# Kernel optimization log

Measured on AMD Instinct MI355X. Metric: run time of the kernel, lower is better.

The kernel has to match this reference:

```python
import jax, jax.numpy as jnp
import numpy as np

B, S, D, F = 8, 2048, 256, 8

def setup_inputs() -> dict:
    key = jax.random.key(0)
    ks = jax.random.split(key, 7)
    hidden_states = jax.random.normal(ks[0], (B, S, D), dtype=jnp.float32)
    # flat indices into zero-prepended [1 + B*S, D] token table; 0 = padding row
    select_idx = jax.random.randint(ks[1], (B, S, F), 0, B * S + 1, dtype=jnp.int32)
    word_mask = jax.random.randint(ks[2], (B, S), 0, 2, dtype=jnp.int32)
    W1 = jax.random.normal(ks[3], (D, D), dtype=jnp.float32) * (1.0 / np.sqrt(D))
    b1 = jax.random.normal(ks[4], (D,), dtype=jnp.float32) * 0.02
    w2 = jax.random.normal(ks[5], (D,), dtype=jnp.float32) * (1.0 / np.sqrt(D))
    b2 = jax.random.normal(ks[6], (1,), dtype=jnp.float32) * 0.02
    return {"hidden_states": hidden_states, "select_idx": select_idx,
            "word_mask": word_mask, "W1": W1, "b1": b1, "w2": w2, "b2": b2}

def reference(hidden_states, select_idx, word_mask, W1, b1, w2, b2):
    b, s, d = hidden_states.shape
    h = jnp.tanh(hidden_states.reshape(-1, d) @ W1.T + b1)          # [B*S, D]
    h = jnp.concatenate([jnp.zeros((1, d), h.dtype), h], axis=0)    # zero padding row at index 0
    g = h[select_idx.reshape(-1)]                                    # gather: [B*S*F, D]
    g = g.reshape(b * s, -1, d).max(axis=1)                          # AdaptiveMaxPool1d(1) over word occurrences
    scores = (g @ w2 + b2[0]).reshape(b, s)                          # w2 linear -> [B, S]
    neg = -10000.0 * (1.0 - word_mask.astype(jnp.float32))
    return scores.astype(jnp.float32) + neg
```

## Files before the change

kernel.cpp:

```cpp
#include <hip/hip_runtime.h>
#include <hip/hip_bf16.h>
#include <math.h>

#define BB 8
#define SS 2048
#define DD 256
#define FF 8
#define NTOK (BB*SS)

typedef __bf16 bf16x8 __attribute__((ext_vector_type(8)));
typedef float  f32x4  __attribute__((ext_vector_type(4)));
typedef float  f32x2  __attribute__((ext_vector_type(2)));

#define BM 32
#define WCH 64
#define NCH (DD/WCH)

__device__ __forceinline__ unsigned pack2_bf16(float a, float b) {
    return (__float_as_uint(a) >> 16) | (__float_as_uint(b) & 0xFFFF0000u);
}
__device__ __forceinline__ float fast_tanh(float x) {
    float e = __expf(2.0f * x);
    return 1.0f - 2.0f * __builtin_amdgcn_rcpf(e + 1.0f);
}
__device__ __forceinline__ unsigned char f32_to_fp8(float v) {
    return (unsigned char)(__builtin_amdgcn_cvt_pk_fp8_f32(v, v, 0, false) & 0xFF);
}

__global__ __launch_bounds__(512, 4) void gemm_tanh_kernel(
    const float* __restrict__ x, const float* __restrict__ W1,
    const float* __restrict__ b1, unsigned char* __restrict__ table)
{
    __shared__ __align__(16) unsigned short xs[BM * DD];
    __shared__ __align__(16) unsigned short wb[WCH * DD];

    const int tid  = threadIdx.x;
    const int bx   = blockIdx.x;
    const int tok0 = bx * BM;

    if (bx == 0 && tid < 64) ((unsigned int*)table)[tid] = 0u;

    const int wave = tid >> 6, lane = tid & 63;
    const int mf = wave >> 2;
    const int nf = wave & 3;
    const int lr = lane & 15;
    const int kg = lane >> 4;
    const int sw = lr & 7;

    f32x4 wr[8];
    auto wload = [&](int nc) {
        #pragma unroll
        for (int p = 0; p < 8; ++p) {
            int s = p * 512 + tid;
            int row = s >> 6, k4 = s & 63;
            wr[p] = *(const f32x4*)&W1[(size_t)(nc * WCH + row) * DD + k4 * 4];
        }
    };
    auto wstore = [&]() {
        #pragma unroll
        for (int p = 0; p < 8; ++p) {
            int s = p * 512 + tid;
            int row = s >> 6, k4 = s & 63;
            uint2 pk;
            pk.x = pack2_bf16(wr[p].x, wr[p].y);
            pk.y = pack2_bf16(wr[p].z, wr[p].w);
            int gp = (k4 >> 1) ^ (row & 7);
            *(uint2*)&wb[row * DD + gp * 8 + (k4 & 1) * 4] = pk;
        }
    };

    wload(0);

    #pragma unroll
    for (int p = 0; p < 4; ++p) {
        int s = p * 512 + tid;
        int row = s >> 6, k4 = s & 63;
        f32x4 v = *(const f32x4*)&x[(size_t)(tok0 + row) * DD + k4 * 4];
        uint2 pk;
        pk.x = pack2_bf16(v.x, v.y);
        pk.y = pack2_bf16(v.z, v.w);
        int gp = (k4 >> 1) ^ (row & 7);
        *(uint2*)&xs[row * DD + gp * 8 + (k4 & 1) * 4] = pk;
    }

    wstore();
    __syncthreads();

    f32x4 acc[NCH];
    #pragma unroll
    for (int nc = 0; nc < NCH; ++nc) acc[nc] = (f32x4){0.f, 0.f, 0.f, 0.f};

    const int arow = mf * 16 + lr;
    const int nrow = nf * 16 + lr;

    #pragma unroll
    for (int nc = 0; nc < NCH; ++nc) {
        if (nc + 1 < NCH) wload(nc + 1);

        #pragma unroll
        for (int c = 0; c < 8; ++c) {
            int gp8 = ((c * 4 + kg) ^ sw) * 8;
            bf16x8 af = *(const bf16x8*)&xs[arow * DD + gp8];
            bf16x8 bf = *(const bf16x8*)&wb[nrow * DD + gp8];
            acc[nc] = __builtin_amdgcn_mfma_f32_16x16x32_bf16(af, bf, acc[nc], 0, 0, 0);
        }
        __syncthreads();
        if (nc + 1 < NCH) {
            wstore();
            __syncthreads();
        }
    }

    float bj[NCH];
    #pragma unroll
    for (int nc = 0; nc < NCH; ++nc) bj[nc] = b1[nc * WCH + nf * 16 + lr];

    unsigned char* sc = (unsigned char*)&xs[0];
    #pragma unroll
    for (int nc = 0; nc < NCH; ++nc) {
        #pragma unroll
        for (int r = 0; r < 4; ++r) {
            int row = mf * 16 + kg * 4 + r;
            int col = nc * WCH + nf * 16 + lr;
            float v = fast_tanh(acc[nc][r] + bj[nc]);
            sc[row * 272 + col] = f32_to_fp8(v);
        }
    }
    __syncthreads();
    {
        int row = tid >> 4;
        int off = (tid & 15) * 16;
        uint4 v = *(const uint4*)&sc[row * 272 + off];
        *(uint4*)&table[(size_t)(1 + tok0 + row) * DD + off] = v;
    }
}

__global__ __launch_bounds__(256) void gather_score_kernel(
    const unsigned char* __restrict__ table,
    const int* __restrict__ select_idx,
    const int* __restrict__ word_mask,
    const float* __restrict__ w2,
    const float* __restrict__ b2,
    float* __restrict__ out)
{
    const int tid  = threadIdx.x;
    const int lane = tid & 63;
    const int wv   = tid >> 6;
    const int i    = blockIdx.x * 4 + wv;
    const int half = lane >> 5;
    const int c    = lane & 31;
    const int d0   = c * 8;

    const int4* sp = (const int4*)(select_idx + (size_t)i * FF);
    int4 q0 = sp[0], q1 = sp[1];
    int rows[4];
    rows[0] = half ? q0.y : q0.x;
    rows[1] = half ? q0.w : q0.z;
    rows[2] = half ? q1.y : q1.x;
    rows[3] = half ? q1.w : q1.z;

    float m[8];
    #pragma unroll
    for (int j = 0; j < 8; ++j) m[j] = -INFINITY;

    #pragma unroll
    for (int it = 0; it < 4; ++it) {
        uint2 u = *(const uint2*)(table + (size_t)rows[it] * DD + d0);
        f32x2 a0 = __builtin_amdgcn_cvt_pk_f32_fp8(u.x, false);
        f32x2 a1 = __builtin_amdgcn_cvt_pk_f32_fp8(u.x, true);
        f32x2 a2 = __builtin_amdgcn_cvt_pk_f32_fp8(u.y, false);
        f32x2 a3 = __builtin_amdgcn_cvt_pk_f32_fp8(u.y, true);
        m[0] = fmaxf(m[0], a0.x); m[1] = fmaxf(m[1], a0.y);
        m[2] = fmaxf(m[2], a1.x); m[3] = fmaxf(m[3], a1.y);
        m[4] = fmaxf(m[4], a2.x); m[5] = fmaxf(m[5], a2.y);
        m[6] = fmaxf(m[6], a3.x); m[7] = fmaxf(m[7], a3.y);
    }

    #pragma unroll
    for (int j = 0; j < 8; ++j) m[j] = fmaxf(m[j], __shfl_xor(m[j], 32));

    f32x4 wa = *(const f32x4*)&w2[d0];
    f32x4 wb = *(const f32x4*)&w2[d0 + 4];
    float p = m[0] * wa.x + m[1] * wa.y + m[2] * wa.z + m[3] * wa.w
            + m[4] * wb.x + m[5] * wb.y + m[6] * wb.z + m[7] * wb.w;

    #pragma unroll
    for (int off = 16; off; off >>= 1) p += __shfl_xor(p, off);

    if (lane == 0) {
        float neg = word_mask[i] ? 0.f : -10000.f;
        out[i] = p + b2[0] + neg;
    }
}

extern "C" void kernel_launch(void* const* d_in, const int* in_sizes, int n_in,
                              void* d_out, int out_size, void* d_ws, size_t ws_size,
                              hipStream_t stream) {
    const float* hs    = (const float*)d_in[0];
    const int*   sidx  = (const int*)  d_in[1];
    const int*   wmask = (const int*)  d_in[2];
    const float* W1    = (const float*)d_in[3];
    const float* b1    = (const float*)d_in[4];
    const float* w2    = (const float*)d_in[5];
    const float* b2    = (const float*)d_in[6];
    float* out = (float*)d_out;

    unsigned char* table = (unsigned char*)d_ws;

    gemm_tanh_kernel<<<NTOK / BM, 512, 0, stream>>>(hs, W1, b1, table);
    gather_score_kernel<<<NTOK / 4, 256, 0, stream>>>(table, sidx, wmask, w2, b2, out);
}
```

Before: 90.51 us.

## Double GEMM token tile and process two tokens per wave in gather

```diff
diff --git a/kernel.cpp b/kernel.cpp
--- a/kernel.cpp
+++ b/kernel.cpp
@@ -12,7 +12,7 @@
 typedef float  f32x4  __attribute__((ext_vector_type(4)));
 typedef float  f32x2  __attribute__((ext_vector_type(2)));
 
-#define BM 32
+#define BM 64
 #define WCH 64
 #define NCH (DD/WCH)
 
@@ -27,12 +27,12 @@
     return (unsigned char)(__builtin_amdgcn_cvt_pk_fp8_f32(v, v, 0, false) & 0xFF);
 }
 
-__global__ __launch_bounds__(512, 4) void gemm_tanh_kernel(
+__global__ __launch_bounds__(1024, 4) void gemm_tanh_kernel(
     const float* __restrict__ x, const float* __restrict__ W1,
     const float* __restrict__ b1, unsigned char* __restrict__ table)
 {
     __shared__ __align__(16) unsigned short xs[BM * DD];
-    __shared__ __align__(16) unsigned short wb[WCH * DD];
+    __shared__ __align__(16) unsigned short wt[WCH * DD];
 
     const int tid  = threadIdx.x;
     const int bx   = blockIdx.x;
@@ -41,31 +41,31 @@
     if (bx == 0 && tid < 64) ((unsigned int*)table)[tid] = 0u;
 
     const int wave = tid >> 6, lane = tid & 63;
-    const int mf = wave >> 2;
-    const int nf = wave & 3;
+    const int wm  = wave >> 2;
+    const int wnf = wave & 3;
     const int lr = lane & 15;
     const int kg = lane >> 4;
     const int sw = lr & 7;
 
-    f32x4 wr[8];
+    f32x4 wr[4];
     auto wload = [&](int nc) {
         #pragma unroll
-        for (int p = 0; p < 8; ++p) {
-            int s = p * 512 + tid;
+        for (int p = 0; p < 4; ++p) {
+            int s = p * 1024 + tid;
             int row = s >> 6, k4 = s & 63;
             wr[p] = *(const f32x4*)&W1[(size_t)(nc * WCH + row) * DD + k4 * 4];
         }
     };
     auto wstore = [&]() {
         #pragma unroll
-        for (int p = 0; p < 8; ++p) {
-            int s = p * 512 + tid;
+        for (int p = 0; p < 4; ++p) {
+            int s = p * 1024 + tid;
             int row = s >> 6, k4 = s & 63;
             uint2 pk;
             pk.x = pack2_bf16(wr[p].x, wr[p].y);
             pk.y = pack2_bf16(wr[p].z, wr[p].w);
             int gp = (k4 >> 1) ^ (row & 7);
-            *(uint2*)&wb[row * DD + gp * 8 + (k4 & 1) * 4] = pk;
+            *(uint2*)&wt[row * DD + gp * 8 + (k4 & 1) * 4] = pk;
         }
     };
 
@@ -73,7 +73,7 @@
 
     #pragma unroll
     for (int p = 0; p < 4; ++p) {
-        int s = p * 512 + tid;
+        int s = p * 1024 + tid;
         int row = s >> 6, k4 = s & 63;
         f32x4 v = *(const f32x4*)&x[(size_t)(tok0 + row) * DD + k4 * 4];
         uint2 pk;
@@ -90,8 +90,8 @@
     #pragma unroll
     for (int nc = 0; nc < NCH; ++nc) acc[nc] = (f32x4){0.f, 0.f, 0.f, 0.f};
 
-    const int arow = mf * 16 + lr;
-    const int nrow = nf * 16 + lr;
+    const int arow = wm * 16 + lr;
+    const int nrow = wnf * 16 + lr;
 
     #pragma unroll
     for (int nc = 0; nc < NCH; ++nc) {
@@ -101,7 +101,7 @@
         for (int c = 0; c < 8; ++c) {
             int gp8 = ((c * 4 + kg) ^ sw) * 8;
             bf16x8 af = *(const bf16x8*)&xs[arow * DD + gp8];
-            bf16x8 bf = *(const bf16x8*)&wb[nrow * DD + gp8];
+            bf16x8 bf = *(const bf16x8*)&wt[nrow * DD + gp8];
             acc[nc] = __builtin_amdgcn_mfma_f32_16x16x32_bf16(af, bf, acc[nc], 0, 0, 0);
         }
         __syncthreads();
@@ -113,15 +113,15 @@
 
     float bj[NCH];
     #pragma unroll
-    for (int nc = 0; nc < NCH; ++nc) bj[nc] = b1[nc * WCH + nf * 16 + lr];
+    for (int nc = 0; nc < NCH; ++nc) bj[nc] = b1[nc * WCH + wnf * 16 + lr];
 
     unsigned char* sc = (unsigned char*)&xs[0];
     #pragma unroll
     for (int nc = 0; nc < NCH; ++nc) {
         #pragma unroll
         for (int r = 0; r < 4; ++r) {
-            int row = mf * 16 + kg * 4 + r;
-            int col = nc * WCH + nf * 16 + lr;
+            int row = wm * 16 + kg * 4 + r;
+            int col = nc * WCH + wnf * 16 + lr;
             float v = fast_tanh(acc[nc][r] + bj[nc]);
             sc[row * 272 + col] = f32_to_fp8(v);
         }
@@ -146,50 +146,77 @@
     const int tid  = threadIdx.x;
     const int lane = tid & 63;
     const int wv   = tid >> 6;
-    const int i    = blockIdx.x * 4 + wv;
+    const int iA   = blockIdx.x * 8 + wv * 2;
+    const int iB   = iA + 1;
     const int half = lane >> 5;
     const int c    = lane & 31;
     const int d0   = c * 8;
 
-    const int4* sp = (const int4*)(select_idx + (size_t)i * FF);
-    int4 q0 = sp[0], q1 = sp[1];
-    int rows[4];
-    rows[0] = half ? q0.y : q0.x;
-    rows[1] = half ? q0.w : q0.z;
-    rows[2] = half ? q1.y : q1.x;
-    rows[3] = half ? q1.w : q1.z;
-
-    float m[8];
-    #pragma unroll
-    for (int j = 0; j < 8; ++j) m[j] = -INFINITY;
-
+    const int4* spA = (const int4*)(select_idx + (size_t)iA * FF);
+    const int4* spB = (const int4*)(select_idx + (size_t)iB * FF);
+    int4 qa0 = spA[0], qa1 = spA[1];
+    int4 qb0 = spB[0], qb1 = spB[1];
+    int rA[4], rB[4];
+    rA[0] = half ? qa0.y : qa0.x;  rA[1] = half ? qa0.w : qa0.z;
+    rA[2] = half ? qa1.y : qa1.x;  rA[3] = half ? qa1.w : qa1.z;
+    rB[0] = half ? qb0.y : qb0.x;  rB[1] = half ? qb0.w : qb0.z;
+    rB[2] = half ? qb1.y : qb1.x;  rB[3] = half ? qb1.w : qb1.z;
+
+    uint2 uA[4], uB[4];
     #pragma unroll
     for (int it = 0; it < 4; ++it) {
-        uint2 u = *(const uint2*)(table + (size_t)rows[it] * DD + d0);
-        f32x2 a0 = __builtin_amdgcn_cvt_pk_f32_fp8(u.x, false);
-        f32x2 a1 = __builtin_amdgcn_cvt_pk_f32_fp8(u.x, true);
-        f32x2 a2 = __builtin_amdgcn_cvt_pk_f32_fp8(u.y, false);
-        f32x2 a3 = __builtin_amdgcn_cvt_pk_f32_fp8(u.y, true);
-        m[0] = fmaxf(m[0], a0.x); m[1] = fmaxf(m[1], a0.y);
-        m[2] = fmaxf(m[2], a1.x); m[3] = fmaxf(m[3], a1.y);
-        m[4] = fmaxf(m[4], a2.x); m[5] = fmaxf(m[5], a2.y);
-        m[6] = fmaxf(m[6], a3.x); m[7] = fmaxf(m[7], a3.y);
-    }
-
-    #pragma unroll
-    for (int j = 0; j < 8; ++j) m[j] = fmaxf(m[j], __shfl_xor(m[j], 32));
+        uA[it] = *(const uint2*)(table + (size_t)rA[it] * DD + d0);
+        uB[it] = *(const uint2*)(table + (size_t)rB[it] * DD + d0);
+    }
+
+    float mA[8], mB[8];
+    #pragma unroll
+    for (int j = 0; j < 8; ++j) { mA[j] = -INFINITY; mB[j] = -INFINITY; }
+
+    #pragma unroll
+    for (int it = 0; it < 4; ++it) {
+        f32x2 a0 = __builtin_amdgcn_cvt_pk_f32_fp8(uA[it].x, false);
+        f32x2 a1 = __builtin_amdgcn_cvt_pk_f32_fp8(uA[it].x, true);
+        f32x2 a2 = __builtin_amdgcn_cvt_pk_f32_fp8(uA[it].y, false);
+        f32x2 a3 = __builtin_amdgcn_cvt_pk_f32_fp8(uA[it].y, true);
+        mA[0] = fmaxf(mA[0], a0.x); mA[1] = fmaxf(mA[1], a0.y);
+        mA[2] = fmaxf(mA[2], a1.x); mA[3] = fmaxf(mA[3], a1.y);
+        mA[4] = fmaxf(mA[4], a2.x); mA[5] = fmaxf(mA[5], a2.y);
+        mA[6] = fmaxf(mA[6], a3.x); mA[7] = fmaxf(mA[7], a3.y);
+        f32x2 b0 = __builtin_amdgcn_cvt_pk_f32_fp8(uB[it].x, false);
+        f32x2 b1v = __builtin_amdgcn_cvt_pk_f32_fp8(uB[it].x, true);
+        f32x2 b2v = __builtin_amdgcn_cvt_pk_f32_fp8(uB[it].y, false);
+        f32x2 b3 = __builtin_amdgcn_cvt_pk_f32_fp8(uB[it].y, true);
+        mB[0] = fmaxf(mB[0], b0.x); mB[1] = fmaxf(mB[1], b0.y);
+        mB[2] = fmaxf(mB[2], b1v.x); mB[3] = fmaxf(mB[3], b1v.y);
+        mB[4] = fmaxf(mB[4], b2v.x); mB[5] = fmaxf(mB[5], b2v.y);
+        mB[6] = fmaxf(mB[6], b3.x); mB[7] = fmaxf(mB[7], b3.y);
+    }
+
+    #pragma unroll
+    for (int j = 0; j < 8; ++j) {
+        mA[j] = fmaxf(mA[j], __shfl_xor(mA[j], 32));
+        mB[j] = fmaxf(mB[j], __shfl_xor(mB[j], 32));
+    }
 
     f32x4 wa = *(const f32x4*)&w2[d0];
     f32x4 wb = *(const f32x4*)&w2[d0 + 4];
-    float p = m[0] * wa.x + m[1] * wa.y + m[2] * wa.z + m[3] * wa.w
-            + m[4] * wb.x + m[5] * wb.y + m[6] * wb.z + m[7] * wb.w;
-
-    #pragma unroll
-    for (int off = 16; off; off >>= 1) p += __shfl_xor(p, off);
+    float pA = mA[0] * wa.x + mA[1] * wa.y + mA[2] * wa.z + mA[3] * wa.w
+             + mA[4] * wb.x + mA[5] * wb.y + mA[6] * wb.z + mA[7] * wb.w;
+    float pB = mB[0] * wa.x + mB[1] * wa.y + mB[2] * wa.z + mB[3] * wa.w
+             + mB[4] * wb.x + mB[5] * wb.y + mB[6] * wb.z + mB[7] * wb.w;
+
+    #pragma unroll
+    for (int off = 16; off; off >>= 1) {
+        pA += __shfl_xor(pA, off);
+        pB += __shfl_xor(pB, off);
+    }
 
     if (lane == 0) {
-        float neg = word_mask[i] ? 0.f : -10000.f;
-        out[i] = p + b2[0] + neg;
+        float negA = word_mask[iA] ? 0.f : -10000.f;
+        float negB = word_mask[iB] ? 0.f : -10000.f;
+        out[iA] = pA + b2[0] + negA;
+        out[iB] = pB + b2[0] + negB;
     }
 }
 
@@ -207,6 +234,6 @@
 
     unsigned char* table = (unsigned char*)d_ws;
 
-    gemm_tanh_kernel<<<NTOK / BM, 512, 0, stream>>>(hs, W1, b1, table);
-    gather_score_kernel<<<NTOK / 4, 256, 0, stream>>>(table, sidx, wmask, w2, b2, out);
-}
+    gemm_tanh_kernel<<<NTOK / BM, 1024, 0, stream>>>(hs, W1, b1, table);
+    gather_score_kernel<<<NTOK / 8, 256, 0, stream>>>(table, sidx, wmask, w2, b2, out);
+}
```

Measured after the change: 89.53 us. About the same (-1.1%).
